# Performance work log

Measured on AMD Instinct MI355X. Metric: run time of the kernel, lower is better.

## Reference

```python
import jax, jax.numpy as jnp
import numpy as np

N_HEAD = 16
D_HEAD = 64


def setup_inputs() -> dict:
    key = jax.random.key(0)
    k1, k2, k3, k4 = jax.random.split(key, 4)
    T, B, D = 1024, 8, 1024
    input = jax.random.normal(k1, (T, B, D), dtype=jnp.float32)
    pos_enc = jax.random.normal(k2, (T, B, D), dtype=jnp.float32) * 0.1
    # causal mask: True = masked (future positions), broadcast over batch
    causal = jnp.triu(jnp.ones((T, T), dtype=bool), k=1)
    attn_mask = jnp.broadcast_to(causal[None, :, :], (B, T, T))
    W_qkv = jax.random.normal(k3, (D, 3 * N_HEAD * D_HEAD), dtype=jnp.float32) * (D ** -0.5)
    W_o = jax.random.normal(k4, (N_HEAD * D_HEAD, N_HEAD * D_HEAD), dtype=jnp.float32) * ((N_HEAD * D_HEAD) ** -0.5)
    return {"input": input, "pos_enc": pos_enc, "attn_mask": attn_mask,
            "W_qkv": W_qkv, "W_o": W_o}


def reference(input, pos_enc, attn_mask, W_qkv, W_o):
    T, B, D = input.shape
    scale = 1.0 / (D_HEAD ** 0.5)
    # attn_type == 2: qkv on (w + r)
    heads = (input + pos_enc) @ W_qkv                      # [T,B,3*n*d]
    q, k, v = jnp.split(heads, 3, axis=-1)
    q = q.reshape(T, B, N_HEAD, D_HEAD)
    k = k.reshape(T, B, N_HEAD, D_HEAD)
    v = v.reshape(T, B, N_HEAD, D_HEAD)
    # scores [B, n, qlen, klen]
    score = jnp.einsum('ibnd,jbnd->bnij', q, k) * scale
    score = jnp.where(attn_mask[:, None, :, :], -jnp.inf, score)
    prob = jax.nn.softmax(score.astype(jnp.float32), axis=-1)  # [B,n,i,j]
    # coverage: mean over heads -> [B,i,j], then transpose -> [B,j,i]
    coverage = jnp.mean(prob, axis=1).transpose(0, 2, 1)
    # dropout is identity at eval (dropatt=0)
    attn_vec = jnp.einsum('bnij,jbnd->ibnd', prob, v)       # [T,B,n,d]
    attn_vec = attn_vec.reshape(T, B, N_HEAD * D_HEAD)
    attn_out = attn_vec @ W_o
    return attn_out, coverage
```

## Files before the change

kernel.cpp:

```cpp
#include <hip/hip_runtime.h>
#include <hip/hip_bf16.h>


typedef __bf16 v8bf __attribute__((ext_vector_type(8)));
typedef float  v4f  __attribute__((ext_vector_type(4)));
typedef unsigned short v8us __attribute__((ext_vector_type(8)));

#define MFMA16x16x32(a, b, c) __builtin_amdgcn_mfma_f32_16x16x32_bf16(a, b, c, 0, 0, 0)

__device__ __forceinline__ unsigned short f2bf(float f) {
    unsigned int u = __float_as_uint(f);
    u = (u + 0x7FFF + ((u >> 16) & 1)) >> 16;
    return (unsigned short)u;
}

__global__ __launch_bounds__(256) void prep_x(const float* __restrict__ in,
                                              const float* __restrict__ pe,
                                              unsigned short* __restrict__ x) {
    size_t idx = ((size_t)blockIdx.x * 256 + threadIdx.x) * 8;
    v4f a0 = *(const v4f*)(in + idx);
    v4f a1 = *(const v4f*)(in + idx + 4);
    v4f p0 = *(const v4f*)(pe + idx);
    v4f p1 = *(const v4f*)(pe + idx + 4);
    v8us r;
    unsigned short* rp = (unsigned short*)&r;
#pragma unroll
    for (int q = 0; q < 4; q++) {
        rp[q]     = f2bf(a0[q] + p0[q]);
        rp[q + 4] = f2bf(a1[q] + p1[q]);
    }
    *(v8us*)(x + idx) = r;
}

__global__ __launch_bounds__(256) void transpose_f32_bf16(const float* __restrict__ src,
                                                          unsigned short* __restrict__ dst,
                                                          int R, int C) {
    __shared__ alignas(16) unsigned short t[64][72];
    int c0 = blockIdx.x * 64, r0 = blockIdx.y * 64;
    int tid = threadIdx.x;
    int rr = tid >> 2, cg = (tid & 3) * 16;
    const float* s = src + (size_t)(r0 + rr) * C + c0 + cg;
#pragma unroll
    for (int q4 = 0; q4 < 4; q4++) {
        v4f v = *(const v4f*)(s + q4 * 4);
#pragma unroll
        for (int q = 0; q < 4; q++) t[rr][cg + q4 * 4 + q] = f2bf(v[q]);
    }
    __syncthreads();
    v8us o0, o1;
    unsigned short* o0p = (unsigned short*)&o0;
    unsigned short* o1p = (unsigned short*)&o1;
#pragma unroll
    for (int q = 0; q < 8; q++) {
        o0p[q] = t[cg + q][rr];
        o1p[q] = t[cg + 8 + q][rr];
    }
    *(v8us*)(dst + (size_t)(c0 + rr) * R + r0 + cg)     = o0;
    *(v8us*)(dst + (size_t)(c0 + rr) * R + r0 + cg + 8) = o1;
}

__global__ __launch_bounds__(256) void transpose_v(const unsigned short* __restrict__ heads,
                                                   unsigned short* __restrict__ Vt) {
    __shared__ alignas(16) unsigned short t[64][72];
    const int bn = blockIdx.y, b = bn >> 4, n = bn & 15;
    const int j0 = blockIdx.x * 64;
    const int tid = threadIdx.x;
    const int jr = tid >> 2, dg = (tid & 3) * 16;
    const unsigned short* s = heads + ((size_t)(j0 + jr) * 8 + b) * 3072 + 2048 + n * 64 + dg;
    *(v8us*)&t[jr][dg]     = *(const v8us*)(s);
    *(v8us*)&t[jr][dg + 8] = *(const v8us*)(s + 8);
    __syncthreads();
    const int dr = tid >> 2, jg = (tid & 3) * 16;
    v8us o0, o1;
    unsigned short* o0p = (unsigned short*)&o0;
    unsigned short* o1p = (unsigned short*)&o1;
#pragma unroll
    for (int q = 0; q < 8; q++) {
        o0p[q] = t[jg + q][dr];
        o1p[q] = t[jg + 8 + q][dr];
    }
    unsigned short* d = Vt + ((size_t)bn * 64 + dr) * 1024 + j0 + jg;
    *(v8us*)(d)     = o0;
    *(v8us*)(d + 8) = o1;
}

template <bool F32OUT>
__global__ __launch_bounds__(256) void gemm_bf16(const unsigned short* __restrict__ A,
                                                 const unsigned short* __restrict__ Bt,
                                                 void* __restrict__ Cout,
                                                 int M, int N, int K) {
    __shared__ alignas(16) unsigned short As[128][40];
    __shared__ alignas(16) unsigned short Bs[128][40];
    const int tid = threadIdx.x;
    const int lane = tid & 63, wave = tid >> 6;
    const int quad = lane >> 4, lq = lane & 15;
    const int m0 = blockIdx.y * 128, n0 = blockIdx.x * 128;
    const int mW = (wave & 1) * 64, nW = (wave >> 1) * 64;

    v4f acc[4][4];
#pragma unroll
    for (int mi = 0; mi < 4; mi++)
#pragma unroll
        for (int ni = 0; ni < 4; ni++) acc[mi][ni] = (v4f){0.f, 0.f, 0.f, 0.f};

    const int srow = tid >> 1, shalf = (tid & 1) * 16;
    const unsigned short* ag = A  + (size_t)(m0 + srow) * K + shalf;
    const unsigned short* bg = Bt + (size_t)(n0 + srow) * K + shalf;

    for (int k0 = 0; k0 < K; k0 += 32) {
        v8us a0 = *(const v8us*)(ag + k0);
        v8us a1 = *(const v8us*)(ag + k0 + 8);
        v8us b0 = *(const v8us*)(bg + k0);
        v8us b1 = *(const v8us*)(bg + k0 + 8);
        __syncthreads();
        *(v8us*)&As[srow][shalf]     = a0;
        *(v8us*)&As[srow][shalf + 8] = a1;
        *(v8us*)&Bs[srow][shalf]     = b0;
        *(v8us*)&Bs[srow][shalf + 8] = b1;
        __syncthreads();
        v8bf af[4], bfr[4];
#pragma unroll
        for (int mi = 0; mi < 4; mi++) af[mi]  = *(const v8bf*)&As[mW + mi * 16 + lq][quad * 8];
#pragma unroll
        for (int ni = 0; ni < 4; ni++) bfr[ni] = *(const v8bf*)&Bs[nW + ni * 16 + lq][quad * 8];
#pragma unroll
        for (int mi = 0; mi < 4; mi++)
#pragma unroll
            for (int ni = 0; ni < 4; ni++)
                acc[mi][ni] = MFMA16x16x32(af[mi], bfr[ni], acc[mi][ni]);
    }

#pragma unroll
    for (int mi = 0; mi < 4; mi++)
#pragma unroll
        for (int ni = 0; ni < 4; ni++)
#pragma unroll
            for (int r = 0; r < 4; r++) {
                int row = m0 + mW + mi * 16 + quad * 4 + r;
                int col = n0 + nW + ni * 16 + lq;
                if (F32OUT)
                    ((float*)Cout)[(size_t)row * N + col] = acc[mi][ni][r];
                else
                    ((unsigned short*)Cout)[(size_t)row * N + col] = f2bf(acc[mi][ni][r]);
            }
}

#define AT_T  1024
#define AT_B  8
#define AT_NH 16
#define AT_HS 3072
#define AT_ALPHA 0.18033688011112042f

__global__ __launch_bounds__(256) void attn_fused5(const unsigned short* __restrict__ heads,
                                                   const unsigned short* __restrict__ Vt,
                                                   unsigned short* __restrict__ av,
                                                   float* __restrict__ lBuf) {
    __shared__ alignas(16) unsigned short KL[64 * 64];
    __shared__ alignas(16) unsigned short VL[64 * 64];
    __shared__ alignas(16) unsigned short Ps[4 * 16 * 32];
    const int bn = blockIdx.x, b = bn >> 4, n = bn & 15;
    const int y = blockIdx.y;
    const int g = (y < 8) ? (15 - y) : (y - 8);
    const int tid = threadIdx.x;
    const int wv = tid >> 6, lane = tid & 63;
    const int quad = lane >> 4, lq = lane & 15;
    const int i0 = g * 64 + wv * 16;
    const int imax = i0 + 15;

    size_t qbase = ((size_t)(i0 + lq) * 8 + b) * AT_HS + n * 64 + quad * 8;
    v8bf q0 = *(const v8bf*)(heads + qbase);
    v8bf q1 = *(const v8bf*)(heads + qbase + 32);

    const int srow = tid >> 3, sunit = tid & 7;
    const size_t kRowStride = (size_t)8 * AT_HS;
    const unsigned short* kg = heads + ((size_t)srow * 8 + b) * AT_HS + 1024 + n * 64 + sunit * 8;
    const unsigned short* vg = Vt + ((size_t)bn * 64 + srow) * 1024 + sunit * 8;
    const int swz = ((sunit ^ (srow & 7)) * 8);
    unsigned short* kw0 = KL + srow * 64 + swz;
    unsigned short* kw1 = KL + (srow + 32) * 64 + swz;
    unsigned short* vw0 = VL + srow * 64 + swz;
    unsigned short* vw1 = VL + (srow + 32) * 64 + swz;

    v8us kr0 = *(const v8us*)(kg);
    v8us kr1 = *(const v8us*)(kg + 32 * kRowStride);
    v8us vr0 = *(const v8us*)(vg);
    v8us vr1 = *(const v8us*)(vg + 32 * 1024);

    unsigned short* psw = Ps + wv * 512;
    const v8bf* pr = (const v8bf*)(psw + lq * 32 + ((quad ^ (lq & 3)) * 8));
    const int lq7 = lq & 7, lqh = lq >> 3;

    float Sl[4] = {0.f, 0.f, 0.f, 0.f};
    v4f o[4];
#pragma unroll
    for (int dt = 0; dt < 4; dt++) o[dt] = (v4f){0.f, 0.f, 0.f, 0.f};

    for (int c = 0; c <= g; ++c) {
        __syncthreads();
        *(v8us*)kw0 = kr0; *(v8us*)kw1 = kr1;
        *(v8us*)vw0 = vr0; *(v8us*)vw1 = vr1;
        __syncthreads();
        if (c < g) {
            const unsigned short* kgn = kg + (size_t)(c + 1) * 64 * kRowStride;
            kr0 = *(const v8us*)(kgn);
            kr1 = *(const v8us*)(kgn + 32 * kRowStride);
            const unsigned short* vgn = vg + (c + 1) * 64;
            vr0 = *(const v8us*)(vgn);
            vr1 = *(const v8us*)(vgn + 32 * 1024);
        }
        const int jb = c * 64;
#pragma unroll
        for (int jj = 0; jj < 64; jj += 32) {
            const int j0 = jb + jj;
            if (j0 <= imax) {
                const v8bf ka = *(const v8bf*)(KL + (jj + lq) * 64      + ((quad ^ lq7) * 8));
                const v8bf kb = *(const v8bf*)(KL + (jj + lq) * 64      + (((4 + quad) ^ lq7) * 8));
                const v8bf kc = *(const v8bf*)(KL + (jj + 16 + lq) * 64 + ((quad ^ lq7) * 8));
                const v8bf kd = *(const v8bf*)(KL + (jj + 16 + lq) * 64 + (((4 + quad) ^ lq7) * 8));
                v4f s0 = (v4f){0.f, 0.f, 0.f, 0.f}, s1 = s0;
                s0 = MFMA16x16x32(q0, ka, s0);
                s0 = MFMA16x16x32(q1, kb, s0);
                s1 = MFMA16x16x32(q0, kc, s1);
                s1 = MFMA16x16x32(q1, kd, s1);
                const int ja = j0 + lq, jb2 = j0 + 16 + lq;
#pragma unroll
                for (int r = 0; r < 4; ++r) {
                    const int i = i0 + quad * 4 + r;
                    float e0 = exp2f(s0[r] * AT_ALPHA);
                    float e1 = exp2f(s1[r] * AT_ALPHA);
                    float p0 = (ja  <= i) ? e0 : 0.f;
                    float p1 = (jb2 <= i) ? e1 : 0.f;
                    Sl[r] += p0 + p1;
                    psw[(quad * 4 + r) * 32 + ((lqh ^ r) * 8) + lq7]        = f2bf(p0);
                    psw[(quad * 4 + r) * 32 + (((lqh | 2) ^ r) * 8) + lq7]  = f2bf(p1);
                }
                const v8bf pf = *pr;
#pragma unroll
                for (int dt = 0; dt < 4; ++dt) {
                    const v8bf vf = *(const v8bf*)(VL + (dt * 16 + lq) * 64 +
                                                   ((((jj >> 3) + quad) ^ lq7) * 8));
                    o[dt] = MFMA16x16x32(pf, vf, o[dt]);
                }
            }
        }
    }

#pragma unroll
    for (int mask = 1; mask < 16; mask <<= 1)
#pragma unroll
        for (int r = 0; r < 4; r++)
            Sl[r] += __shfl_xor(Sl[r], mask);
    float linv[4];
#pragma unroll
    for (int r = 0; r < 4; r++) linv[r] = __builtin_amdgcn_rcpf(Sl[r]);
    if (lq == 0) {
#pragma unroll
        for (int r = 0; r < 4; r++) {
            int i = i0 + quad * 4 + r;
            lBuf[(size_t)bn * AT_T + i] = Sl[r];
        }
    }
#pragma unroll
    for (int dt = 0; dt < 4; dt++)
#pragma unroll
        for (int r = 0; r < 4; r++) {
            int i = i0 + quad * 4 + r;
            av[((size_t)i * 8 + b) * 1024 + n * 64 + dt * 16 + lq] = f2bf(o[dt][r] * linv[r]);
        }
}

__global__ __launch_bounds__(256) void coverage3(const unsigned short* __restrict__ heads,
                                                 const float* __restrict__ lBuf,
                                                 float* __restrict__ cov) {
    const int jt64 = blockIdx.x, it64 = blockIdx.y, b = blockIdx.z;
    const int i0 = it64 * 64, j0 = jt64 * 64;
    const int tid = threadIdx.x;

    if (jt64 > it64) {
        float* base = cov + (size_t)b * 1048576 + (size_t)(j0 + (tid >> 2)) * 1024
                      + i0 + (tid & 3) * 16;
        v4f z = (v4f){0.f, 0.f, 0.f, 0.f};
#pragma unroll
        for (int q = 0; q < 4; q++) *(v4f*)(base + q * 4) = z;
        return;
    }

    __shared__ alignas(16) char smem[64 * 68 * 4];
    unsigned short* QL = (unsigned short*)smem;
    unsigned short* KL = (unsigned short*)(smem + 8192);
    float* TF = (float*)smem;

    const int wv = tid >> 6, lane = tid & 63;
    const int quad = lane >> 4, lq = lane & 15, lq7 = lq & 7;
    const bool diag = (it64 == jt64);
    const int jtmax = diag ? wv : 3;

    const int srow = tid >> 3, sunit = tid & 7;
    const unsigned short* qgb = heads + ((size_t)(i0 + srow) * 8 + b) * AT_HS + sunit * 8;
    const unsigned short* kgb = heads + ((size_t)(j0 + srow) * 8 + b) * AT_HS + 1024 + sunit * 8;
    const int rowOff32 = 32 * 8 * AT_HS;
    const int swz = (sunit ^ (srow & 7)) * 8;
    unsigned short* qw0 = QL + srow * 64 + swz;
    unsigned short* qw1 = QL + (srow + 32) * 64 + swz;
    unsigned short* kw0 = KL + srow * 64 + swz;
    unsigned short* kw1 = KL + (srow + 32) * 64 + swz;

    v8us qr0 = *(const v8us*)(qgb);
    v8us qr1 = *(const v8us*)(qgb + rowOff32);
    v8us kr0 = *(const v8us*)(kgb);
    v8us kr1 = *(const v8us*)(kgb + rowOff32);

    v4f acc[4];
#pragma unroll
    for (int jt = 0; jt < 4; jt++) acc[jt] = (v4f){0.f, 0.f, 0.f, 0.f};

    const float* lrow = lBuf + (size_t)b * 16 * AT_T + i0 + wv * 16 + quad * 4;

    for (int n = 0; n < 16; ++n) {
        __syncthreads();
        *(v8us*)qw0 = qr0; *(v8us*)qw1 = qr1;
        *(v8us*)kw0 = kr0; *(v8us*)kw1 = kr1;
        __syncthreads();
        if (n < 15) {
            qr0 = *(const v8us*)(qgb + (n + 1) * 64);
            qr1 = *(const v8us*)(qgb + (n + 1) * 64 + rowOff32);
            kr0 = *(const v8us*)(kgb + (n + 1) * 64);
            kr1 = *(const v8us*)(kgb + (n + 1) * 64 + rowOff32);
        }
        v4f lv = *(const v4f*)(lrow + (size_t)n * AT_T);
        float linv[4];
#pragma unroll
        for (int r = 0; r < 4; r++) linv[r] = __builtin_amdgcn_rcpf(lv[r]);

        const v8bf qa = *(const v8bf*)(QL + (wv * 16 + lq) * 64 + ((quad ^ lq7) * 8));
        const v8bf qb = *(const v8bf*)(QL + (wv * 16 + lq) * 64 + (((4 + quad) ^ lq7) * 8));
#pragma unroll
        for (int jt = 0; jt < 4; jt++) {
            if (jt <= jtmax) {
                const v8bf ka = *(const v8bf*)(KL + (jt * 16 + lq) * 64 + ((quad ^ lq7) * 8));
                const v8bf kb = *(const v8bf*)(KL + (jt * 16 + lq) * 64 + (((4 + quad) ^ lq7) * 8));
                v4f s = (v4f){0.f, 0.f, 0.f, 0.f};
                s = MFMA16x16x32(qa, ka, s);
                s = MFMA16x16x32(qb, kb, s);
#pragma unroll
                for (int r = 0; r < 4; r++) {
                    float e = exp2f(s[r] * AT_ALPHA);
                    if (diag && jt == wv && lq > quad * 4 + r) e = 0.f;
                    acc[jt][r] = fmaf(e, linv[r], acc[jt][r]);
                }
            }
        }
    }

    __syncthreads();
#pragma unroll
    for (int jt = 0; jt < 4; jt++) {
        v4f w = acc[jt] * 0.0625f;
        *(v4f*)(TF + (size_t)(jt * 16 + lq) * 68 + wv * 16 + quad * 4) = w;
    }
    __syncthreads();
    {
        const int jl = tid >> 2, cg = (tid & 3) * 16;
        float* dst = cov + (size_t)b * 1048576 + (size_t)(j0 + jl) * 1024 + i0 + cg;
        const float* src = TF + (size_t)jl * 68 + cg;
#pragma unroll
        for (int q = 0; q < 4; q++) *(v4f*)(dst + q * 4) = *(const v4f*)(src + q * 4);
    }
}

extern "C" void kernel_launch(void* const* d_in, const int* in_sizes, int n_in,
                              void* d_out, int out_size, void* d_ws, size_t ws_size,
                              hipStream_t stream) {
    const float* input = (const float*)d_in[0];
    const float* pos   = (const float*)d_in[1];
    const float* Wqkv  = (const float*)d_in[3];
    const float* Wo    = (const float*)d_in[4];
    float* out = (float*)d_out;

    char* ws = (char*)d_ws;
    if (ws_size < 93323264) return;
    unsigned short* x     = (unsigned short*)(ws);
    unsigned short* heads = (unsigned short*)(ws + 16777216);
    unsigned short* av    = (unsigned short*)(ws + 67108864);
    unsigned short* WqkvT = (unsigned short*)(ws + 83886080);
    unsigned short* WoT   = (unsigned short*)(ws + 90177536);
    float* lBuf = (float*)(ws + 92798976);
    unsigned short* Vt = x;

    prep_x<<<4096, 256, 0, stream>>>(input, pos, x);
    transpose_f32_bf16<<<dim3(48, 16), 256, 0, stream>>>(Wqkv, WqkvT, 1024, 3072);
    transpose_f32_bf16<<<dim3(16, 16), 256, 0, stream>>>(Wo, WoT, 1024, 1024);
    gemm_bf16<false><<<dim3(24, 64), 256, 0, stream>>>(x, WqkvT, heads, 8192, 3072, 1024);
    transpose_v<<<dim3(16, 128), 256, 0, stream>>>(heads, Vt);
    attn_fused5<<<dim3(128, 16), 256, 0, stream>>>(heads, Vt, av, lBuf);
    coverage3<<<dim3(16, 16, 8), 256, 0, stream>>>(heads, lBuf, out + 8388608);
    gemm_bf16<true><<<dim3(8, 64), 256, 0, stream>>>(av, WoT, out, 8192, 1024, 1024);
}
```

Before: 363.0 us.

## Rewrite bf16 GEMM with direct global-to-LDS loads, XOR swizzle, K=64 tiles, XCD remap

The two projection GEMMs now use global_load_lds to copy tiles straight into shared memory, skipping the register staging step. The LDS layout is XOR-swizzled so fragment reads avoid bank conflicts, the K step grows from 32 to 64 per barrier pair, and block IDs are remapped across 8 groups so neighbouring tiles share L2 on the XCDs. Together these aim to cut load latency, LDS conflicts and barrier overhead. The risks are that there is still no double buffering, and that the remap assumes the block count divides by 8.

```diff
diff --git a/kernel.cpp b/kernel.cpp
--- a/kernel.cpp
+++ b/kernel.cpp
@@ -7,6 +7,10 @@
 typedef unsigned short v8us __attribute__((ext_vector_type(8)));
 
 #define MFMA16x16x32(a, b, c) __builtin_amdgcn_mfma_f32_16x16x32_bf16(a, b, c, 0, 0, 0)
+
+#define GLD_LDS16(g, l) \
+    __builtin_amdgcn_global_load_lds((const __attribute__((address_space(1))) void*)(g), \
+                                     (__attribute__((address_space(3))) void*)(l), 16, 0, 0)
 
 __device__ __forceinline__ unsigned short f2bf(float f) {
     unsigned int u = __float_as_uint(f);
@@ -85,16 +89,22 @@
 }
 
 template <bool F32OUT>
-__global__ __launch_bounds__(256) void gemm_bf16(const unsigned short* __restrict__ A,
-                                                 const unsigned short* __restrict__ Bt,
-                                                 void* __restrict__ Cout,
-                                                 int M, int N, int K) {
-    __shared__ alignas(16) unsigned short As[128][40];
-    __shared__ alignas(16) unsigned short Bs[128][40];
+__global__ __launch_bounds__(256) void gemm_bf16_v2(const unsigned short* __restrict__ A,
+                                                    const unsigned short* __restrict__ Bt,
+                                                    void* __restrict__ Cout,
+                                                    int M, int N, int K) {
+    __shared__ alignas(16) unsigned short As[128 * 64];
+    __shared__ alignas(16) unsigned short Bs[128 * 64];
+
+    const int nwgx = gridDim.x;
+    const int id   = blockIdx.y * nwgx + blockIdx.x;
+    const int cpx  = (nwgx * gridDim.y) >> 3;
+    const int id2  = (id & 7) * cpx + (id >> 3);
+    const int m0 = (id2 / nwgx) * 128, n0 = (id2 % nwgx) * 128;
+
     const int tid = threadIdx.x;
     const int lane = tid & 63, wave = tid >> 6;
-    const int quad = lane >> 4, lq = lane & 15;
-    const int m0 = blockIdx.y * 128, n0 = blockIdx.x * 128;
+    const int quad = lane >> 4, lq = lane & 15, lq7 = lq & 7;
     const int mW = (wave & 1) * 64, nW = (wave >> 1) * 64;
 
     v4f acc[4][4];
@@ -103,31 +113,36 @@
 #pragma unroll
         for (int ni = 0; ni < 4; ni++) acc[mi][ni] = (v4f){0.f, 0.f, 0.f, 0.f};
 
-    const int srow = tid >> 1, shalf = (tid & 1) * 16;
-    const unsigned short* ag = A  + (size_t)(m0 + srow) * K + shalf;
-    const unsigned short* bg = Bt + (size_t)(n0 + srow) * K + shalf;
-
-    for (int k0 = 0; k0 < K; k0 += 32) {
-        v8us a0 = *(const v8us*)(ag + k0);
-        v8us a1 = *(const v8us*)(ag + k0 + 8);
-        v8us b0 = *(const v8us*)(bg + k0);
-        v8us b1 = *(const v8us*)(bg + k0 + 8);
-        __syncthreads();
-        *(v8us*)&As[srow][shalf]     = a0;
-        *(v8us*)&As[srow][shalf + 8] = a1;
-        *(v8us*)&Bs[srow][shalf]     = b0;
-        *(v8us*)&Bs[srow][shalf + 8] = b1;
-        __syncthreads();
-        v8bf af[4], bfr[4];
-#pragma unroll
-        for (int mi = 0; mi < 4; mi++) af[mi]  = *(const v8bf*)&As[mW + mi * 16 + lq][quad * 8];
-#pragma unroll
-        for (int ni = 0; ni < 4; ni++) bfr[ni] = *(const v8bf*)&Bs[nW + ni * 16 + lq][quad * 8];
-#pragma unroll
-        for (int mi = 0; mi < 4; mi++)
+    const int lr = lane >> 3, lu = lane & 7;
+    const int ug = lu ^ lr;
+    const unsigned short* agl = A  + (size_t)(m0 + wave * 32 + lr) * K + ug * 8;
+    const unsigned short* bgl = Bt + (size_t)(n0 + wave * 32 + lr) * K + ug * 8;
+    unsigned short* AsW = (unsigned short*)As + wave * 32 * 64;
+    unsigned short* BsW = (unsigned short*)Bs + wave * 32 * 64;
+
+    for (int k0 = 0; k0 < K; k0 += 64) {
+        __syncthreads();
+#pragma unroll
+        for (int t = 0; t < 4; t++) {
+            GLD_LDS16(agl + k0 + (size_t)t * 8 * K, AsW + t * 512);
+            GLD_LDS16(bgl + k0 + (size_t)t * 8 * K, BsW + t * 512);
+        }
+        __syncthreads();
+#pragma unroll
+        for (int h = 0; h < 2; h++) {
+            v8bf af[4], bfr[4];
+#pragma unroll
+            for (int mi = 0; mi < 4; mi++)
+                af[mi] = *(const v8bf*)&As[(mW + mi * 16 + lq) * 64 + (((quad + 4 * h) ^ lq7) * 8)];
 #pragma unroll
             for (int ni = 0; ni < 4; ni++)
-                acc[mi][ni] = MFMA16x16x32(af[mi], bfr[ni], acc[mi][ni]);
+                bfr[ni] = *(const v8bf*)&Bs[(nW + ni * 16 + lq) * 64 + (((quad + 4 * h) ^ lq7) * 8)];
+#pragma unroll
+            for (int mi = 0; mi < 4; mi++)
+#pragma unroll
+                for (int ni = 0; ni < 4; ni++)
+                    acc[mi][ni] = MFMA16x16x32(af[mi], bfr[ni], acc[mi][ni]);
+        }
     }
 
 #pragma unroll
@@ -390,9 +405,9 @@
     prep_x<<<4096, 256, 0, stream>>>(input, pos, x);
     transpose_f32_bf16<<<dim3(48, 16), 256, 0, stream>>>(Wqkv, WqkvT, 1024, 3072);
     transpose_f32_bf16<<<dim3(16, 16), 256, 0, stream>>>(Wo, WoT, 1024, 1024);
-    gemm_bf16<false><<<dim3(24, 64), 256, 0, stream>>>(x, WqkvT, heads, 8192, 3072, 1024);
+    gemm_bf16_v2<false><<<dim3(24, 64), 256, 0, stream>>>(x, WqkvT, heads, 8192, 3072, 1024);
     transpose_v<<<dim3(16, 128), 256, 0, stream>>>(heads, Vt);
     attn_fused5<<<dim3(128, 16), 256, 0, stream>>>(heads, Vt, av, lBuf);
     coverage3<<<dim3(16, 16, 8), 256, 0, stream>>>(heads, lBuf, out + 8388608);
-    gemm_bf16<true><<<dim3(8, 64), 256, 0, stream>>>(av, WoT, out, 8192, 1024, 1024);
-}
+    gemm_bf16_v2<true><<<dim3(8, 64), 256, 0, stream>>>(av, WoT, out, 8192, 1024, 1024);
+}
```

Result: faster. 337.8 us (-6.9%).
